# Kernel optimization log

Measured on AMD Instinct MI355X. Metric: run time of the kernel, lower is better.

The kernel has to match this reference:

```python
import jax, jax.numpy as jnp
import numpy as np

BETA = 0.25  # args.beta
B, T, D, K = 16, 4096, 64, 1024


def setup_inputs() -> dict:
    key = jax.random.key(0)
    kz, kw = jax.random.split(key)
    z = jax.random.normal(kz, (B, T, D), dtype=jnp.float32)
    # nn.Embedding weight init: uniform(-1/K, 1/K)
    emb = jax.random.uniform(kw, (K, D), dtype=jnp.float32,
                             minval=-1.0 / K, maxval=1.0 / K)
    return {"z": z, "emb": emb}


def reference(z, emb):
    # z: [B, T, D] (torch code loops over first dim; all elements non-empty here)
    # emb: [K, D] codebook
    b, t, d = z.shape
    zf = z.reshape(-1, d)                                   # [B*T, D]
    # squared euclidean distances: ||z||^2 + ||e||^2 - 2 z.e
    dist = (jnp.sum(zf * zf, axis=1, keepdims=True)
            + jnp.sum(emb * emb, axis=1)
            - 2.0 * zf @ emb.T)                             # [B*T, K]
    idx = jnp.argmin(dist, axis=1).reshape(b, t)            # [B, T] int
    z_q_raw = emb[idx]                                      # [B, T, D] gather
    sg = jax.lax.stop_gradient
    # per-batch-element means, summed (loop accumulates loss per z_t)
    commit = jnp.mean((sg(z_q_raw) - z) ** 2, axis=(1, 2))  # [B]
    codebk = jnp.mean((z_q_raw - sg(z)) ** 2, axis=(1, 2))  # [B]
    loss = jnp.sum(BETA * commit + codebk)
    # straight-through estimator
    z_q = z + sg(z_q_raw - z)
    return z_q, loss, idx
```

## Files before the change

kernel.cpp:

```cpp
#include <hip/hip_runtime.h>
#include <math.h>
#include <float.h>

#define NROWS    65536
#define DD       64
#define KK       1024
#define LOSS_OFF 4194304
#define IDX_OFF  4194305
#define RPB      128
#define MAXC     32
#define TPR      8
#define NRND     8

typedef short  short8 __attribute__((ext_vector_type(8)));
typedef float  f32x4  __attribute__((ext_vector_type(4)));

__device__ __forceinline__ void async_copy16(void* lds, const void* g) {
    __builtin_amdgcn_global_load_lds(
        (const __attribute__((address_space(1))) unsigned int*)g,
        (__attribute__((address_space(3))) unsigned int*)lds, 16, 0, 0);
}

__device__ __forceinline__ unsigned short bf16rne(float x) {
    unsigned int u = __float_as_uint(x);
    return (unsigned short)((u + 0x7fffu + ((u >> 16) & 1u)) >> 16);
}

__device__ __forceinline__ float np_sumsq64_stream(const float* p) {
#pragma clang fp contract(off)
    float r[8];
    {
        const float4 u0 = *reinterpret_cast<const float4*>(p);
        const float4 u1 = *reinterpret_cast<const float4*>(p + 4);
        r[0] = u0.x * u0.x; r[1] = u0.y * u0.y; r[2] = u0.z * u0.z; r[3] = u0.w * u0.w;
        r[4] = u1.x * u1.x; r[5] = u1.y * u1.y; r[6] = u1.z * u1.z; r[7] = u1.w * u1.w;
    }
#pragma unroll
    for (int i = 8; i < 64; i += 8) {
        const float4 u0 = *reinterpret_cast<const float4*>(p + i);
        const float4 u1 = *reinterpret_cast<const float4*>(p + i + 4);
        r[0] += u0.x * u0.x; r[1] += u0.y * u0.y; r[2] += u0.z * u0.z; r[3] += u0.w * u0.w;
        r[4] += u1.x * u1.x; r[5] += u1.y * u1.y; r[6] += u1.z * u1.z; r[7] += u1.w * u1.w;
    }
    return ((r[0] + r[1]) + (r[2] + r[3])) + ((r[4] + r[5]) + (r[6] + r[7]));
}

__global__ void vq_prep(const float* __restrict__ emb,
                        float* __restrict__ bn,
                        unsigned short* __restrict__ ebf) {
#pragma clang fp contract(off)
    const int gtid = blockIdx.x * 256 + threadIdx.x;
    const int code = gtid >> 3;
    const int j    = gtid & 7;
    const float* ep = emb + (size_t)code * DD;
    float r = 0.f;
#pragma unroll
    for (int i = 0; i < 8; ++i) {
        const float v = ep[8 * i + j];
        r += v * v;
    }
    const float s1 = r  + __shfl_xor(r,  1, 64);
    const float s2 = s1 + __shfl_xor(s1, 2, 64);
    const float s3 = s2 + __shfl_xor(s2, 4, 64);
    if (j == 0) bn[code] = s3;

    const float* cp = emb + (size_t)gtid * 8;
    const float4 u0 = *reinterpret_cast<const float4*>(cp);
    const float4 u1 = *reinterpret_cast<const float4*>(cp + 4);
    short8 s;
    s[0] = (short)bf16rne(u0.x); s[1] = (short)bf16rne(u0.y);
    s[2] = (short)bf16rne(u0.z); s[3] = (short)bf16rne(u0.w);
    s[4] = (short)bf16rne(u1.x); s[5] = (short)bf16rne(u1.y);
    s[6] = (short)bf16rne(u1.z); s[7] = (short)bf16rne(u1.w);
    *reinterpret_cast<short8*>(ebf + (size_t)gtid * 8) = s;
}

__global__ __launch_bounds__(256)
void vq_main(const float* __restrict__ z, const float* __restrict__ emb,
             const unsigned short* __restrict__ ebf,
             const float* __restrict__ bn, float* __restrict__ out) {
    __shared__ char  dbuf[2][TPR * 2048] __attribute__((aligned(16)));
    __shared__ float a_s[RPB];
    __shared__ float bn_s[KK];
    __shared__ int   cnt[RPB];
    __shared__ int   clist[RPB][MAXC];
    __shared__ int   bidx[RPB];

    const int tid  = threadIdx.x;
    const int lane = tid & 63;
    const int wv   = __builtin_amdgcn_readfirstlane(tid) >> 6;
    const int q    = lane >> 4;
    const int c16  = lane & 15;
    const int rowbase = blockIdx.x * RPB;

    const char* sbase = (const char*)ebf + (size_t)c16 * 128 + (size_t)q * 16;

    if (tid < RPB) {
        a_s[tid] = np_sumsq64_stream(z + (size_t)(rowbase + tid) * DD);
        cnt[tid] = 0;
    }
    {
        const int i = tid * 4;
        *reinterpret_cast<float4*>(&bn_s[i]) =
            *reinterpret_cast<const float4*>(bn + i);
    }

    short8 afr[2][2];
#pragma unroll
    for (int rt = 0; rt < 2; ++rt) {
#pragma unroll
        for (int kh = 0; kh < 2; ++kh) {
            const float* zp = z + (size_t)(rowbase + 32 * wv + 16 * rt + c16) * DD
                              + 32 * kh + 8 * q;
            const float4 u0 = *reinterpret_cast<const float4*>(zp);
            const float4 u1 = *reinterpret_cast<const float4*>(zp + 4);
            short8 s;
            s[0] = (short)bf16rne(u0.x); s[1] = (short)bf16rne(u0.y);
            s[2] = (short)bf16rne(u0.z); s[3] = (short)bf16rne(u0.w);
            s[4] = (short)bf16rne(u1.x); s[5] = (short)bf16rne(u1.y);
            s[6] = (short)bf16rne(u1.z); s[7] = (short)bf16rne(u1.w);
            afr[rt][kh] = s;
        }
    }

    auto stage = [&](int R, int buf) {
        const char* s0 = sbase + (size_t)(TPR * R + 2 * wv) * 2048;
        char* d = &dbuf[buf][(2 * wv) * 2048 + lane * 16];
        async_copy16(d,               s0);
        async_copy16(d + 1024,        s0 + 64);
        async_copy16(d + 2048,        s0 + 2048);
        async_copy16(d + 2048 + 1024, s0 + 2048 + 64);
    };

    float mn[8], T[8], Wr[8];
#pragma unroll
    for (int i = 0; i < 8; ++i) { mn[i] = FLT_MAX; T[i] = -FLT_MAX; }

    stage(0, 0);
    __syncthreads();

#pragma unroll
    for (int i = 0; i < 8; ++i) {
        const int rowl = 32 * wv + 16 * (i >> 2) + 4 * q + (i & 3);
        Wr[i] = 1.8e-4f * sqrtf(a_s[rowl]) + 1.2e-4f;
    }

    auto proc = [&](int cur, int j, int colbase, bool update, bool collect) {
        const char* tb = &dbuf[cur][j * 2048 + lane * 16];
        const short8 b0 = *reinterpret_cast<const short8*>(tb);
        const short8 b1 = *reinterpret_cast<const short8*>(tb + 1024);
        f32x4 acc0 = {0.f, 0.f, 0.f, 0.f};
        f32x4 acc1 = {0.f, 0.f, 0.f, 0.f};
        acc0 = __builtin_amdgcn_mfma_f32_16x16x32_bf16(afr[0][0], b0, acc0, 0, 0, 0);
        acc0 = __builtin_amdgcn_mfma_f32_16x16x32_bf16(afr[0][1], b1, acc0, 0, 0, 0);
        acc1 = __builtin_amdgcn_mfma_f32_16x16x32_bf16(afr[1][0], b0, acc1, 0, 0, 0);
        acc1 = __builtin_amdgcn_mfma_f32_16x16x32_bf16(afr[1][1], b1, acc1, 0, 0, 0);
        const int col = colbase + c16;
        const float bnv = bn_s[col];
#pragma unroll
        for (int r = 0; r < 4; ++r) {
            const float d0 = fmaf(-2.f, acc0[r], bnv);
            const float d1 = fmaf(-2.f, acc1[r], bnv);
            if (update) {
                mn[r]     = fminf(mn[r],     d0);
                mn[4 + r] = fminf(mn[4 + r], d1);
            }
            if (collect) {
                if (d0 <= T[r]) {
                    const int rowl = 32 * wv + 4 * q + r;
                    const int slot = atomicAdd(&cnt[rowl], 1);
                    if (slot < MAXC) clist[rowl][slot] = col;
                }
                if (d1 <= T[4 + r]) {
                    const int rowl = 32 * wv + 16 + 4 * q + r;
                    const int slot = atomicAdd(&cnt[rowl], 1);
                    if (slot < MAXC) clist[rowl][slot] = col;
                }
            }
        }
    };

    auto fold = [&]() {
#pragma unroll
        for (int mask = 1; mask < 16; mask <<= 1)
#pragma unroll
            for (int i = 0; i < 8; ++i)
                mn[i] = fminf(mn[i], __shfl_xor(mn[i], mask, 64));
#pragma unroll
        for (int i = 0; i < 8; ++i) T[i] = mn[i] + Wr[i];
    };

    for (int R = 0; R < NRND; ++R) {
        const int cur = R & 1;
        if (R < NRND - 1) stage(R + 1, cur ^ 1);
        if (R == 0) {
#pragma unroll
            for (int j = 0; j < TPR; ++j) proc(cur, j, 16 * j, true, false);
            fold();
#pragma unroll
            for (int j = 0; j < TPR; ++j) proc(cur, j, 16 * j, false, true);
        } else {
#pragma unroll
            for (int j = 0; j < TPR; ++j)
                proc(cur, j, 16 * (TPR * R + j), true, true);
            fold();
        }
        __syncthreads();
    }

#pragma unroll
    for (int rt = 0; rt < 2; ++rt) {
        const int rowl = 32 * wv + 16 * rt + c16;
        const int row  = rowbase + rowl;
        const int nc   = cnt[rowl];
        const bool full = nc > MAXC;
        const int lim  = full ? KK : nc;
        const float av = a_s[rowl];
        const float* zp = z + (size_t)row * DD;
        float sb = FLT_MAX;
        int   cb = 0x7fffffff;
        for (int jj = q; jj < lim; jj += 4) {
            const int c = full ? jj : clist[rowl][jj];
            const float* ep = emb + (size_t)c * DD;
            float dot = 0.f;
#pragma unroll
            for (int d = 0; d < DD; d += 4) {
                const float4 zv = *reinterpret_cast<const float4*>(zp + d);
                const float4 ev = *reinterpret_cast<const float4*>(ep + d);
                dot = fmaf(zv.x, ev.x, dot); dot = fmaf(zv.y, ev.y, dot);
                dot = fmaf(zv.z, ev.z, dot); dot = fmaf(zv.w, ev.w, dot);
            }
            const float tt = av + bn_s[c];
            const float sd = fmaf(-2.f, dot, tt);
            if (sd < sb || (sd == sb && c < cb)) { sb = sd; cb = c; }
        }
#pragma unroll
        for (int mask = 16; mask < 64; mask <<= 1) {
            const float so = __shfl_xor(sb, mask, 64);
            const int   co = __shfl_xor(cb, mask, 64);
            if (so < sb || (so == sb && co < cb)) { sb = so; cb = co; }
        }
        if (cb > 1023) cb = 0;
        if (q == 0) bidx[rowl] = cb;
    }
    __syncthreads();

    if (tid >= RPB) return;
    const int row = rowbase + tid;
    const int bid = bidx[tid];
    const float* ep = emb + (size_t)bid * DD;
    const float* zp = z + (size_t)row * DD;
    float* op = out + (size_t)row * DD;
    double sac = 0.0;
#pragma unroll
    for (int d = 0; d < DD; d += 4) {
        const float4 zv = *reinterpret_cast<const float4*>(zp + d);
        const float4 e4 = *reinterpret_cast<const float4*>(ep + d);
        const float df0 = e4.x - zv.x;
        const float df1 = e4.y - zv.y;
        const float df2 = e4.z - zv.z;
        const float df3 = e4.w - zv.w;
        float4 qv;
        qv.x = zv.x + df0; qv.y = zv.y + df1;
        qv.z = zv.z + df2; qv.w = zv.w + df3;
        *reinterpret_cast<float4*>(op + d) = qv;
        sac += (double)(df0 * df0); sac += (double)(df1 * df1);
        sac += (double)(df2 * df2); sac += (double)(df3 * df3);
    }
    out[IDX_OFF + row] = (float)bid;

#pragma unroll
    for (int off = 32; off > 0; off >>= 1) sac += __shfl_down(sac, off, 64);
    if (lane == 0)
        atomicAdd(&out[LOSS_OFF], (float)((1.25 * sac) / 262144.0));
}

extern "C" void kernel_launch(void* const* d_in, const int* in_sizes, int n_in,
                              void* d_out, int out_size, void* d_ws, size_t ws_size,
                              hipStream_t stream) {
    const float* z   = (const float*)d_in[0];
    const float* emb = (const float*)d_in[1];
    float* out = (float*)d_out;

    float*          bnw = (float*)d_ws;
    unsigned short* ebf = (unsigned short*)((char*)d_ws + 4096);

    vq_prep<<<dim3(32), dim3(256), 0, stream>>>(emb, bnw, ebf);
    vq_main<<<dim3(NROWS / RPB), dim3(256), 0, stream>>>(z, emb, ebf, bnw, out);
}
```

Before: 141.4 us.

## Split candidate search into two full passes with smaller row blocks

Halves rows per block (one 16-row MFMA tile per wave) and replaces the single pass with running threshold updates by two passes over the codebook. The first pass computes the exact bf16 minimum, the second collects candidates against a final threshold. This shrinks candidate lists (MAXC 16) and removes per-round shuffle folds, and the smaller per-block footprint lets more blocks run per CU. The cost is streaming the codebook through LDS twice, and each B fragment is now reused across one row tile instead of two.

```diff
diff --git a/kernel.cpp b/kernel.cpp
--- a/kernel.cpp
+++ b/kernel.cpp
@@ -7,10 +7,10 @@
 #define KK       1024
 #define LOSS_OFF 4194304
 #define IDX_OFF  4194305
-#define RPB      128
-#define MAXC     32
-#define TPR      8
-#define NRND     8
+#define RPB      64
+#define MAXC     16
+#define TPR      4
+#define NRND     16
 
 typedef short  short8 __attribute__((ext_vector_type(8)));
 typedef float  f32x4  __attribute__((ext_vector_type(4)));
@@ -94,6 +94,8 @@
     const int rowbase = blockIdx.x * RPB;
 
     const char* sbase = (const char*)ebf + (size_t)c16 * 128 + (size_t)q * 16;
+    char* dst0 = &dbuf[0][wv * 2048 + lane * 16];
+    char* dst1 = &dbuf[1][wv * 2048 + lane * 16];
 
     if (tid < RPB) {
         a_s[tid] = np_sumsq64_stream(z + (size_t)(rowbase + tid) * DD);
@@ -105,112 +107,97 @@
             *reinterpret_cast<const float4*>(bn + i);
     }
 
-    short8 afr[2][2];
-#pragma unroll
-    for (int rt = 0; rt < 2; ++rt) {
-#pragma unroll
-        for (int kh = 0; kh < 2; ++kh) {
-            const float* zp = z + (size_t)(rowbase + 32 * wv + 16 * rt + c16) * DD
-                              + 32 * kh + 8 * q;
-            const float4 u0 = *reinterpret_cast<const float4*>(zp);
-            const float4 u1 = *reinterpret_cast<const float4*>(zp + 4);
-            short8 s;
-            s[0] = (short)bf16rne(u0.x); s[1] = (short)bf16rne(u0.y);
-            s[2] = (short)bf16rne(u0.z); s[3] = (short)bf16rne(u0.w);
-            s[4] = (short)bf16rne(u1.x); s[5] = (short)bf16rne(u1.y);
-            s[6] = (short)bf16rne(u1.z); s[7] = (short)bf16rne(u1.w);
-            afr[rt][kh] = s;
-        }
+    short8 afr[2];
+#pragma unroll
+    for (int kh = 0; kh < 2; ++kh) {
+        const float* zp = z + (size_t)(rowbase + 16 * wv + c16) * DD
+                          + 32 * kh + 8 * q;
+        const float4 u0 = *reinterpret_cast<const float4*>(zp);
+        const float4 u1 = *reinterpret_cast<const float4*>(zp + 4);
+        short8 s;
+        s[0] = (short)bf16rne(u0.x); s[1] = (short)bf16rne(u0.y);
+        s[2] = (short)bf16rne(u0.z); s[3] = (short)bf16rne(u0.w);
+        s[4] = (short)bf16rne(u1.x); s[5] = (short)bf16rne(u1.y);
+        s[6] = (short)bf16rne(u1.z); s[7] = (short)bf16rne(u1.w);
+        afr[kh] = s;
     }
 
     auto stage = [&](int R, int buf) {
-        const char* s0 = sbase + (size_t)(TPR * R + 2 * wv) * 2048;
-        char* d = &dbuf[buf][(2 * wv) * 2048 + lane * 16];
-        async_copy16(d,               s0);
-        async_copy16(d + 1024,        s0 + 64);
-        async_copy16(d + 2048,        s0 + 2048);
-        async_copy16(d + 2048 + 1024, s0 + 2048 + 64);
+        const char* s0 = sbase + (size_t)(TPR * R + wv) * 2048;
+        char* d = buf ? dst1 : dst0;
+        async_copy16(d,        s0);
+        async_copy16(d + 1024, s0 + 64);
     };
 
-    float mn[8], T[8], Wr[8];
-#pragma unroll
-    for (int i = 0; i < 8; ++i) { mn[i] = FLT_MAX; T[i] = -FLT_MAX; }
+    float mn[4];
+#pragma unroll
+    for (int i = 0; i < 4; ++i) mn[i] = FLT_MAX;
 
     stage(0, 0);
     __syncthreads();
 
-#pragma unroll
-    for (int i = 0; i < 8; ++i) {
-        const int rowl = 32 * wv + 16 * (i >> 2) + 4 * q + (i & 3);
-        Wr[i] = 1.8e-4f * sqrtf(a_s[rowl]) + 1.2e-4f;
-    }
-
-    auto proc = [&](int cur, int j, int colbase, bool update, bool collect) {
-        const char* tb = &dbuf[cur][j * 2048 + lane * 16];
-        const short8 b0 = *reinterpret_cast<const short8*>(tb);
-        const short8 b1 = *reinterpret_cast<const short8*>(tb + 1024);
-        f32x4 acc0 = {0.f, 0.f, 0.f, 0.f};
-        f32x4 acc1 = {0.f, 0.f, 0.f, 0.f};
-        acc0 = __builtin_amdgcn_mfma_f32_16x16x32_bf16(afr[0][0], b0, acc0, 0, 0, 0);
-        acc0 = __builtin_amdgcn_mfma_f32_16x16x32_bf16(afr[0][1], b1, acc0, 0, 0, 0);
-        acc1 = __builtin_amdgcn_mfma_f32_16x16x32_bf16(afr[1][0], b0, acc1, 0, 0, 0);
-        acc1 = __builtin_amdgcn_mfma_f32_16x16x32_bf16(afr[1][1], b1, acc1, 0, 0, 0);
-        const int col = colbase + c16;
-        const float bnv = bn_s[col];
-#pragma unroll
-        for (int r = 0; r < 4; ++r) {
-            const float d0 = fmaf(-2.f, acc0[r], bnv);
-            const float d1 = fmaf(-2.f, acc1[r], bnv);
-            if (update) {
-                mn[r]     = fminf(mn[r],     d0);
-                mn[4 + r] = fminf(mn[4 + r], d1);
-            }
-            if (collect) {
+    for (int R = 0; R < NRND; ++R) {
+        const int cur = R & 1;
+        if (R < NRND - 1) stage(R + 1, cur ^ 1);
+#pragma unroll
+        for (int j = 0; j < TPR; ++j) {
+            const char* tb = &dbuf[cur][j * 2048 + lane * 16];
+            const short8 b0 = *reinterpret_cast<const short8*>(tb);
+            const short8 b1 = *reinterpret_cast<const short8*>(tb + 1024);
+            f32x4 acc = {0.f, 0.f, 0.f, 0.f};
+            acc = __builtin_amdgcn_mfma_f32_16x16x32_bf16(afr[0], b0, acc, 0, 0, 0);
+            acc = __builtin_amdgcn_mfma_f32_16x16x32_bf16(afr[1], b1, acc, 0, 0, 0);
+            const float bnv = bn_s[16 * (TPR * R + j) + c16];
+#pragma unroll
+            for (int r = 0; r < 4; ++r)
+                mn[r] = fminf(mn[r], fmaf(-2.f, acc[r], bnv));
+        }
+        __syncthreads();
+    }
+
+#pragma unroll
+    for (int mask = 1; mask < 16; mask <<= 1)
+#pragma unroll
+        for (int i = 0; i < 4; ++i)
+            mn[i] = fminf(mn[i], __shfl_xor(mn[i], mask, 64));
+    float T[4];
+#pragma unroll
+    for (int i = 0; i < 4; ++i) {
+        const int rowl = 16 * wv + 4 * q + i;
+        T[i] = mn[i] + 1.8e-4f * sqrtf(a_s[rowl]) + 1.2e-4f;
+    }
+
+    stage(0, 0);
+    __syncthreads();
+
+    for (int R = 0; R < NRND; ++R) {
+        const int cur = R & 1;
+        if (R < NRND - 1) stage(R + 1, cur ^ 1);
+#pragma unroll
+        for (int j = 0; j < TPR; ++j) {
+            const char* tb = &dbuf[cur][j * 2048 + lane * 16];
+            const short8 b0 = *reinterpret_cast<const short8*>(tb);
+            const short8 b1 = *reinterpret_cast<const short8*>(tb + 1024);
+            f32x4 acc = {0.f, 0.f, 0.f, 0.f};
+            acc = __builtin_amdgcn_mfma_f32_16x16x32_bf16(afr[0], b0, acc, 0, 0, 0);
+            acc = __builtin_amdgcn_mfma_f32_16x16x32_bf16(afr[1], b1, acc, 0, 0, 0);
+            const int col = 16 * (TPR * R + j) + c16;
+            const float bnv = bn_s[col];
+#pragma unroll
+            for (int r = 0; r < 4; ++r) {
+                const float d0 = fmaf(-2.f, acc[r], bnv);
                 if (d0 <= T[r]) {
-                    const int rowl = 32 * wv + 4 * q + r;
-                    const int slot = atomicAdd(&cnt[rowl], 1);
-                    if (slot < MAXC) clist[rowl][slot] = col;
-                }
-                if (d1 <= T[4 + r]) {
-                    const int rowl = 32 * wv + 16 + 4 * q + r;
+                    const int rowl = 16 * wv + 4 * q + r;
                     const int slot = atomicAdd(&cnt[rowl], 1);
                     if (slot < MAXC) clist[rowl][slot] = col;
                 }
             }
         }
-    };
-
-    auto fold = [&]() {
-#pragma unroll
-        for (int mask = 1; mask < 16; mask <<= 1)
-#pragma unroll
-            for (int i = 0; i < 8; ++i)
-                mn[i] = fminf(mn[i], __shfl_xor(mn[i], mask, 64));
-#pragma unroll
-        for (int i = 0; i < 8; ++i) T[i] = mn[i] + Wr[i];
-    };
-
-    for (int R = 0; R < NRND; ++R) {
-        const int cur = R & 1;
-        if (R < NRND - 1) stage(R + 1, cur ^ 1);
-        if (R == 0) {
-#pragma unroll
-            for (int j = 0; j < TPR; ++j) proc(cur, j, 16 * j, true, false);
-            fold();
-#pragma unroll
-            for (int j = 0; j < TPR; ++j) proc(cur, j, 16 * j, false, true);
-        } else {
-#pragma unroll
-            for (int j = 0; j < TPR; ++j)
-                proc(cur, j, 16 * (TPR * R + j), true, true);
-            fold();
-        }
         __syncthreads();
     }
 
-#pragma unroll
-    for (int rt = 0; rt < 2; ++rt) {
-        const int rowl = 32 * wv + 16 * rt + c16;
+    {
+        const int rowl = 16 * wv + c16;
         const int row  = rowbase + rowl;
         const int nc   = cnt[rowl];
         const bool full = nc > MAXC;
```

Result: faster. 126.2 us (-10.7%).
